# Optimization experiments

Hardware: AMD Instinct MI355X
Metric: run time of the kernel (lower is better)

## Reference

```python
import jax, jax.numpy as jnp
import numpy as np

LAGS = 2
SLOPE = 0.2  # leaky_relu negative slope


def setup_inputs() -> dict:
    key = jax.random.key(0)
    ks = jax.random.split(key, 12)
    B, T, D, E, H = 32, 1002, 16, 32, 64  # batch, lags+length, latent, embed, hidden
    s = 0.1
    return {
        "x": jax.random.normal(ks[0], (B, T, D), jnp.float32),
        "embeddings": jax.random.normal(ks[1], (B, T, E), jnp.float32),
        # per-latent-dim stacked MLP2 params (num_layers=3 hidden + output head)
        "W0": jax.random.normal(ks[2], (D, H, E + 1), jnp.float32) * s,
        "b0": jax.random.normal(ks[3], (D, H), jnp.float32) * s,
        "W1": jax.random.normal(ks[4], (D, H, H), jnp.float32) * s,
        "b1": jax.random.normal(ks[5], (D, H), jnp.float32) * s,
        "W2": jax.random.normal(ks[6], (D, H, H), jnp.float32) * s,
        "b2": jax.random.normal(ks[7], (D, H), jnp.float32) * s,
        "Wo": jax.random.normal(ks[8], (D, 1, H), jnp.float32) * s,
        "bo": jax.random.normal(ks[9], (D, 1), jnp.float32) * s,
    }


def reference(x, embeddings, W0, b0, W1, b1, W2, b2, Wo, bo):
    B, TL, D = x.shape
    length = TL - LAGS
    E = embeddings.shape[-1]
    N = B * length

    # last element of each unfolded window == x[:, LAGS:, :]
    x_t = x[:, LAGS:, :].reshape(N, D)                       # [N, D]
    emb = embeddings[:, -length:, :].reshape(N, E)           # [N, E]
    # per-dim input: concat(embedding, x_t[:, i]) -> [N, D, E+1]
    inp = jnp.concatenate(
        [jnp.broadcast_to(emb[:, None, :], (N, D, E)), x_t[:, :, None]], axis=-1
    )

    # batched tiny MLPs across latent dims; keep leaky-relu gates for analytic Jacobian
    z0 = jnp.einsum('dhe,nde->ndh', W0, inp) + b0            # [N, D, H]
    g0 = jnp.where(z0 >= 0, 1.0, SLOPE)
    a0 = z0 * g0
    z1 = jnp.einsum('dij,ndj->ndi', W1, a0) + b1
    g1 = jnp.where(z1 >= 0, 1.0, SLOPE)
    a1 = z1 * g1
    z2 = jnp.einsum('dij,ndj->ndi', W2, a1) + b2
    g2 = jnp.where(z2 >= 0, 1.0, SLOPE)
    a2 = z2 * g2
    res = jnp.einsum('doh,ndh->ndo', Wo, a2)[..., 0] + bo[:, 0]   # [N, D]

    # d residual_i / d x_t_i : propagate last input column through the chain
    t = g0 * W0[:, :, -1]                                    # [N, D, H]
    t = g1 * jnp.einsum('dij,ndj->ndi', W1, t)
    t = g2 * jnp.einsum('dij,ndj->ndi', W2, t)
    dJ = jnp.einsum('doh,ndh->ndo', Wo, t)[..., 0]           # [N, D]

    logabsdet = jnp.sum(jnp.log(jnp.abs(dJ)), axis=-1)       # [N]

    residuals = res.reshape(B, length, D)
    log_abs_det_jacobian = logabsdet.reshape(B, length)
    return residuals, log_abs_det_jacobian
```

## Files before the change

kernel.cpp:

```cpp
#include <hip/hip_runtime.h>

constexpr int   kT    = 1002;
constexpr int   kD    = 16;
constexpr int   kE    = 32;
constexpr int   kH    = 64;
constexpr int   kLen  = kT - 2;
constexpr int   kN    = 32 * kLen;
constexpr float kSlope = 0.2f;
constexpr int   AS    = 68;
constexpr int   kWsDwPerD = 23552;

typedef __attribute__((ext_vector_type(8))) short bf16x8;
typedef __attribute__((ext_vector_type(4))) float f32x4;
typedef __attribute__((ext_vector_type(2))) __fp16 fp16x2;
typedef __attribute__((ext_vector_type(8))) _Float16 f16x8;

__device__ __forceinline__ unsigned rne2(float x0, float x1, float &h0, float &h1) {
    unsigned u0 = __float_as_uint(x0), u1 = __float_as_uint(x1);
    unsigned r0 = u0 + 0x7FFFu + ((u0 >> 16) & 1u);
    unsigned r1 = u1 + 0x7FFFu + ((u1 >> 16) & 1u);
    h0 = __uint_as_float(r0 & 0xFFFF0000u);
    h1 = __uint_as_float(r1 & 0xFFFF0000u);
    return __builtin_amdgcn_perm(r1, r0, 0x07060302u);
}

__device__ __forceinline__ void split3_2(float x0, float x1,
                                         unsigned &p1, unsigned &p2, unsigned &p3) {
    float h0, h1; p1 = rne2(x0, x1, h0, h1);
    float e0 = x0 - h0, e1 = x1 - h1;
    float m0, m1; p2 = rne2(e0, e1, m0, m1);
    float f0 = e0 - m0, f1 = e1 - m1;
    float t0, t1; p3 = rne2(f0, f1, t0, t1);
}

union FragU { unsigned u[4]; bf16x8 v; };

__device__ __forceinline__ void splitA3(const float4 a0, const float4 a1,
                                        bf16x8 &A1, bf16x8 &A2, bf16x8 &A3) {
    FragU U1, U2, U3;
    split3_2(a0.x, a0.y, U1.u[0], U2.u[0], U3.u[0]);
    split3_2(a0.z, a0.w, U1.u[1], U2.u[1], U3.u[1]);
    split3_2(a1.x, a1.y, U1.u[2], U2.u[2], U3.u[2]);
    split3_2(a1.z, a1.w, U1.u[3], U2.u[3], U3.u[3]);
    A1 = U1.v; A2 = U2.v; A3 = U3.v;
}

__device__ __forceinline__ void split2h(float x0, float x1, unsigned &p1, unsigned &p2) {
    fp16x2 h = __builtin_amdgcn_cvt_pkrtz(x0, x1);
    __builtin_memcpy(&p1, &h, 4);
    fp16x2 l = __builtin_amdgcn_cvt_pkrtz(x0 - (float)h[0], x1 - (float)h[1]);
    __builtin_memcpy(&p2, &l, 4);
}

union FragH { unsigned u[4]; f16x8 v; };

__device__ __forceinline__ void splitA2h(const float4 a0, const float4 a1,
                                         f16x8 &A1, f16x8 &A2) {
    FragH U1, U2;
    split2h(a0.x, a0.y, U1.u[0], U2.u[0]);
    split2h(a0.z, a0.w, U1.u[1], U2.u[1]);
    split2h(a1.x, a1.y, U1.u[2], U2.u[2]);
    split2h(a1.z, a1.w, U1.u[3], U2.u[3]);
    A1 = U1.v; A2 = U2.v;
}

__global__ void prep_weights(const float* __restrict__ W0, const float* __restrict__ W1,
                             const float* __restrict__ W2, unsigned* __restrict__ ws,
                             float* __restrict__ out_ld) {
    int id = blockIdx.x * blockDim.x + threadIdx.x;
    if (id < kN) out_ld[id] = 0.f;
    if (id >= 16 * 9216) return;
    int d = id / 9216, rem = id - d * 9216;
    unsigned* wd = ws + (size_t)d * kWsDwPerD;

    if (rem < 5120) {
        float x0, x1; unsigned o1, o2, o3;
        if (rem < 1024) {
            int idx = rem, j2 = idx & 3, ln = (idx >> 2) & 63, nt = (idx >> 8) & 3;
            int n_ = nt * 16 + (ln & 15), k_ = ((ln >> 4) << 3) + 2 * j2;
            const float* g = W0 + (size_t)d * kH * 33;
            x0 = g[n_ * 33 + k_]; x1 = g[n_ * 33 + k_ + 1];
            o1 = idx; o2 = 1024 + idx; o3 = 2048 + idx;
        } else if (rem < 3072) {
            int idx = rem - 1024, j2 = idx & 3, ln = (idx >> 2) & 63;
            int kt = (idx >> 8) & 1, nt = (idx >> 9) & 3;
            int n_ = nt * 16 + (ln & 15), k_ = kt * 32 + ((ln >> 4) << 3) + 2 * j2;
            const float* g = W1 + (size_t)d * kH * kH;
            x0 = g[n_ * 64 + k_]; x1 = g[n_ * 64 + k_ + 1];
            o1 = 3072 + idx; o2 = 5120 + idx; o3 = 7168 + idx;
        } else {
            int idx = rem - 3072, j2 = idx & 3, ln = (idx >> 2) & 63;
            int kt = (idx >> 8) & 1, nt = (idx >> 9) & 3;
            int n_ = nt * 16 + (ln & 15), k_ = kt * 32 + ((ln >> 4) << 3) + 2 * j2;
            const float* g = W2 + (size_t)d * kH * kH;
            x0 = g[n_ * 64 + k_]; x1 = g[n_ * 64 + k_ + 1];
            o1 = 9216 + idx; o2 = 11264 + idx; o3 = 13312 + idx;
        }
        unsigned p1, p2, p3; split3_2(x0, x1, p1, p2, p3);
        wd[o1] = p1; wd[o2] = p2; wd[o3] = p3;
    } else {
        int idx, base; const float* g;
        if (rem < 7168) { idx = rem - 5120; base = 15360; g = W1 + (size_t)d * kH * kH; }
        else            { idx = rem - 7168; base = 19456; g = W2 + (size_t)d * kH * kH; }
        int j2 = idx & 3, ln = (idx >> 2) & 63;
        int kt = (idx >> 8) & 1, nt = (idx >> 9) & 3;
        int n_ = nt * 16 + (ln & 15), k_ = kt * 32 + ((ln >> 4) << 3) + 2 * j2;
        float x0 = g[n_ * 64 + k_], x1 = g[n_ * 64 + k_ + 1];
        unsigned p1, p2; split2h(x0, x1, p1, p2);
        wd[base + idx] = p1; wd[base + 2048 + idx] = p2;
    }
}

#define MFMA(A, B, C)  __builtin_amdgcn_mfma_f32_16x16x32_bf16((A), (B), (C), 0, 0, 0)
#define MFMAH(A, B, C) __builtin_amdgcn_mfma_f32_16x16x32_f16((A), (B), (C), 0, 0, 0)

__device__ __forceinline__ void layer64_f(f32x4 acc[2][4],
                                          const float* r0, const float* r1,
                                          const unsigned* w1, const unsigned* w2,
                                          const unsigned* w3, int lane, int q) {
    #pragma unroll
    for (int kt = 0; kt < 2; ++kt) {
        bf16x8 A1[2], A2[2], A3[2];
        {
            const float4 a0 = *(const float4*)(r0 + kt * 32 + q * 8);
            const float4 a1 = *(const float4*)(r0 + kt * 32 + q * 8 + 4);
            splitA3(a0, a1, A1[0], A2[0], A3[0]);
            const float4 b0_ = *(const float4*)(r1 + kt * 32 + q * 8);
            const float4 b1_ = *(const float4*)(r1 + kt * 32 + q * 8 + 4);
            splitA3(b0_, b1_, A1[1], A2[1], A3[1]);
        }
        bf16x8 B[4];
        #pragma unroll
        for (int nt = 0; nt < 4; ++nt) B[nt] = *(const bf16x8*)(w1 + (((nt * 2 + kt) * 64 + lane) << 2));
        #pragma unroll
        for (int nt = 0; nt < 4; ++nt)
            #pragma unroll
            for (int mt = 0; mt < 2; ++mt) {
                acc[mt][nt] = MFMA(A3[mt], B[nt], acc[mt][nt]);
                acc[mt][nt] = MFMA(A2[mt], B[nt], acc[mt][nt]);
                acc[mt][nt] = MFMA(A1[mt], B[nt], acc[mt][nt]);
            }
        #pragma unroll
        for (int nt = 0; nt < 4; ++nt) B[nt] = *(const bf16x8*)(w2 + (((nt * 2 + kt) * 64 + lane) << 2));
        #pragma unroll
        for (int nt = 0; nt < 4; ++nt)
            #pragma unroll
            for (int mt = 0; mt < 2; ++mt) {
                acc[mt][nt] = MFMA(A2[mt], B[nt], acc[mt][nt]);
                acc[mt][nt] = MFMA(A1[mt], B[nt], acc[mt][nt]);
            }
        #pragma unroll
        for (int nt = 0; nt < 4; ++nt) B[nt] = *(const bf16x8*)(w3 + (((nt * 2 + kt) * 64 + lane) << 2));
        #pragma unroll
        for (int nt = 0; nt < 4; ++nt)
            #pragma unroll
            for (int mt = 0; mt < 2; ++mt)
                acc[mt][nt] = MFMA(A1[mt], B[nt], acc[mt][nt]);
    }
}

__device__ __forceinline__ void layer64_jh(f32x4 acc[2][4],
                                           const float* r0, const float* r1,
                                           const unsigned* wl1, const unsigned* wl2,
                                           int lane, int q) {
    #pragma unroll
    for (int kt = 0; kt < 2; ++kt) {
        f16x8 A1[2], A2[2];
        {
            const float4 a0 = *(const float4*)(r0 + kt * 32 + q * 8);
            const float4 a1 = *(const float4*)(r0 + kt * 32 + q * 8 + 4);
            splitA2h(a0, a1, A1[0], A2[0]);
            const float4 b0_ = *(const float4*)(r1 + kt * 32 + q * 8);
            const float4 b1_ = *(const float4*)(r1 + kt * 32 + q * 8 + 4);
            splitA2h(b0_, b1_, A1[1], A2[1]);
        }
        f16x8 B[4];
        #pragma unroll
        for (int nt = 0; nt < 4; ++nt) B[nt] = *(const f16x8*)(wl1 + (((nt * 2 + kt) * 64 + lane) << 2));
        #pragma unroll
        for (int nt = 0; nt < 4; ++nt)
            #pragma unroll
            for (int mt = 0; mt < 2; ++mt) {
                acc[mt][nt] = MFMAH(A2[mt], B[nt], acc[mt][nt]);
                acc[mt][nt] = MFMAH(A1[mt], B[nt], acc[mt][nt]);
            }
        #pragma unroll
        for (int nt = 0; nt < 4; ++nt) B[nt] = *(const f16x8*)(wl2 + (((nt * 2 + kt) * 64 + lane) << 2));
        #pragma unroll
        for (int nt = 0; nt < 4; ++nt)
            #pragma unroll
            for (int mt = 0; mt < 2; ++mt)
                acc[mt][nt] = MFMAH(A1[mt], B[nt], acc[mt][nt]);
    }
}

__global__ __launch_bounds__(128, 2) void np_mfma_kernel(
    const float* __restrict__ x, const float* __restrict__ emb,
    const float* __restrict__ W0, const float* __restrict__ b0,
    const float* __restrict__ b1, const float* __restrict__ b2,
    const float* __restrict__ Wo, const float* __restrict__ bo,
    const unsigned* __restrict__ ws,
    float* __restrict__ out_res, float* __restrict__ out_ld)
{
    __shared__ __align__(16) float act[64 * AS];

    const int tid  = threadIdx.x;
    const int lane = tid & 63;
    const int wave = __builtin_amdgcn_readfirstlane(tid >> 6);
    const int c = lane & 15, q = lane >> 4;
    const int tb = wave * 32;
    const int d  = blockIdx.y;
    const int nW = blockIdx.x * 64 + tb;

    const int nX  = nW + ((q >> 1) << 4) + c;
    const int bbX = nX / kLen;
    const float xm = x[((size_t)(bbX * kT + (nX - bbX * kLen) + 2)) * kD + d];
    float xr[2][4];
    #pragma unroll
    for (int mt = 0; mt < 2; ++mt)
        #pragma unroll
        for (int r = 0; r < 4; ++r)
            xr[mt][r] = __shfl(xm, mt * 32 + q * 4 + r, 64);

    const float* W0g = W0 + (size_t)d * kH * 33;
    float b0v[4], wov[4], w0xv[4];
    #pragma unroll
    for (int nt = 0; nt < 4; ++nt) {
        const int u = nt * 16 + c;
        b0v[nt]  = b0[d * kH + u];
        wov[nt]  = Wo[d * kH + u];
        w0xv[nt] = W0g[u * 33 + 32];
    }
    const float bov = bo[d];
    const unsigned* wd = ws + (size_t)d * kWsDwPerD;
    const float* r0 = &act[(tb + c) * AS];
    const float* r1 = &act[(tb + 16 + c) * AS];

    unsigned m0 = 0, m1 = 0, m2 = 0;
    f32x4 acc[2][4];

    {
        bf16x8 A1[2], A2[2], A3[2];
        #pragma unroll
        for (int mt = 0; mt < 2; ++mt) {
            const int nA = nW + mt * 16 + c;
            const int bb = nA / kLen;
            const size_t src = (size_t)(bb * kT + (nA - bb * kLen) + 2);
            const float4* ep = (const float4*)(emb + src * kE + q * 8);
            splitA3(ep[0], ep[1], A1[mt], A2[mt], A3[mt]);
        }
        #pragma unroll
        for (int mt = 0; mt < 2; ++mt)
            #pragma unroll
            for (int nt = 0; nt < 4; ++nt) {
                f32x4 a;
                #pragma unroll
                for (int r = 0; r < 4; ++r) a[r] = fmaf(xr[mt][r], w0xv[nt], b0v[nt]);
                acc[mt][nt] = a;
            }
        bf16x8 B[4];
        #pragma unroll
        for (int nt = 0; nt < 4; ++nt) B[nt] = *(const bf16x8*)(wd + ((nt * 64 + lane) << 2));
        #pragma unroll
        for (int nt = 0; nt < 4; ++nt)
            #pragma unroll
            for (int mt = 0; mt < 2; ++mt) {
                acc[mt][nt] = MFMA(A3[mt], B[nt], acc[mt][nt]);
                acc[mt][nt] = MFMA(A2[mt], B[nt], acc[mt][nt]);
                acc[mt][nt] = MFMA(A1[mt], B[nt], acc[mt][nt]);
            }
        #pragma unroll
        for (int nt = 0; nt < 4; ++nt) B[nt] = *(const bf16x8*)(wd + 1024 + ((nt * 64 + lane) << 2));
        #pragma unroll
        for (int nt = 0; nt < 4; ++nt)
            #pragma unroll
            for (int mt = 0; mt < 2; ++mt) {
                acc[mt][nt] = MFMA(A2[mt], B[nt], acc[mt][nt]);
                acc[mt][nt] = MFMA(A1[mt], B[nt], acc[mt][nt]);
            }
        #pragma unroll
        for (int nt = 0; nt < 4; ++nt) B[nt] = *(const bf16x8*)(wd + 2048 + ((nt * 64 + lane) << 2));
        #pragma unroll
        for (int nt = 0; nt < 4; ++nt)
            #pragma unroll
            for (int mt = 0; mt < 2; ++mt)
                acc[mt][nt] = MFMA(A1[mt], B[nt], acc[mt][nt]);
        #pragma unroll
        for (int mt = 0; mt < 2; ++mt)
            #pragma unroll
            for (int nt = 0; nt < 4; ++nt)
                #pragma unroll
                for (int r = 0; r < 4; ++r) {
                    float z = acc[mt][nt][r];
                    m0 |= (unsigned)(z >= 0.f) << (mt * 16 + nt * 4 + r);
                    act[(tb + mt * 16 + q * 4 + r) * AS + nt * 16 + c] = fmaxf(z, z * kSlope);
                }
    }

    {
        #pragma unroll
        for (int nt = 0; nt < 4; ++nt) {
            const float bv = b1[d * kH + nt * 16 + c];
            #pragma unroll
            for (int mt = 0; mt < 2; ++mt) {
                f32x4 a;
                #pragma unroll
                for (int r = 0; r < 4; ++r) a[r] = bv;
                acc[mt][nt] = a;
            }
        }
        layer64_f(acc, r0, r1, wd + 3072, wd + 5120, wd + 7168, lane, q);
        #pragma unroll
        for (int mt = 0; mt < 2; ++mt)
            #pragma unroll
            for (int nt = 0; nt < 4; ++nt)
                #pragma unroll
                for (int r = 0; r < 4; ++r) {
                    float z = acc[mt][nt][r];
                    m1 |= (unsigned)(z >= 0.f) << (mt * 16 + nt * 4 + r);
                    act[(tb + mt * 16 + q * 4 + r) * AS + nt * 16 + c] = fmaxf(z, z * kSlope);
                }
    }

    {
        #pragma unroll
        for (int nt = 0; nt < 4; ++nt) {
            const float bv = b2[d * kH + nt * 16 + c];
            #pragma unroll
            for (int mt = 0; mt < 2; ++mt) {
                f32x4 a;
                #pragma unroll
                for (int r = 0; r < 4; ++r) a[r] = bv;
                acc[mt][nt] = a;
            }
        }
        layer64_f(acc, r0, r1, wd + 9216, wd + 11264, wd + 13312, lane, q);
        float pr[2][4] = {{0.f,0.f,0.f,0.f},{0.f,0.f,0.f,0.f}};
        #pragma unroll
        for (int mt = 0; mt < 2; ++mt)
            #pragma unroll
            for (int nt = 0; nt < 4; ++nt)
                #pragma unroll
                for (int r = 0; r < 4; ++r) {
                    float z = acc[mt][nt][r];
                    m2 |= (unsigned)(z >= 0.f) << (mt * 16 + nt * 4 + r);
                    pr[mt][r] = fmaf(wov[nt], fmaxf(z, z * kSlope), pr[mt][r]);
                }
        #pragma unroll
        for (int mt = 0; mt < 2; ++mt)
            #pragma unroll
            for (int r = 0; r < 4; ++r) {
                #pragma unroll
                for (int s = 1; s < 16; s <<= 1) pr[mt][r] += __shfl_xor(pr[mt][r], s, 16);
            }
        if (c == 0) {
            #pragma unroll
            for (int mt = 0; mt < 2; ++mt)
                #pragma unroll
                for (int r = 0; r < 4; ++r)
                    out_res[(size_t)(nW + mt * 16 + q * 4 + r) * kD + d] = pr[mt][r] + bov;
        }
    }

    #pragma unroll
    for (int mt = 0; mt < 2; ++mt)
        #pragma unroll
        for (int nt = 0; nt < 4; ++nt)
            #pragma unroll
            for (int r = 0; r < 4; ++r)
                act[(tb + mt * 16 + q * 4 + r) * AS + nt * 16 + c] =
                    (((m0 >> (mt * 16 + nt * 4 + r)) & 1u) ? 1.f : kSlope) * w0xv[nt];

    {
        #pragma unroll
        for (int mt = 0; mt < 2; ++mt)
            #pragma unroll
            for (int nt = 0; nt < 4; ++nt) acc[mt][nt] = (f32x4){0.f, 0.f, 0.f, 0.f};
        layer64_jh(acc, r0, r1, wd + 15360, wd + 17408, lane, q);
        #pragma unroll
        for (int mt = 0; mt < 2; ++mt)
            #pragma unroll
            for (int nt = 0; nt < 4; ++nt)
                #pragma unroll
                for (int r = 0; r < 4; ++r)
                    act[(tb + mt * 16 + q * 4 + r) * AS + nt * 16 + c] =
                        (((m1 >> (mt * 16 + nt * 4 + r)) & 1u) ? 1.f : kSlope) * acc[mt][nt][r];
    }

    {
        #pragma unroll
        for (int mt = 0; mt < 2; ++mt)
            #pragma unroll
            for (int nt = 0; nt < 4; ++nt) acc[mt][nt] = (f32x4){0.f, 0.f, 0.f, 0.f};
        layer64_jh(acc, r0, r1, wd + 19456, wd + 21504, lane, q);
        float pr[2][4] = {{0.f,0.f,0.f,0.f},{0.f,0.f,0.f,0.f}};
        #pragma unroll
        for (int mt = 0; mt < 2; ++mt)
            #pragma unroll
            for (int nt = 0; nt < 4; ++nt)
                #pragma unroll
                for (int r = 0; r < 4; ++r) {
                    float t = (((m2 >> (mt * 16 + nt * 4 + r)) & 1u) ? 1.f : kSlope) * acc[mt][nt][r];
                    pr[mt][r] = fmaf(wov[nt], t, pr[mt][r]);
                }
        #pragma unroll
        for (int mt = 0; mt < 2; ++mt)
            #pragma unroll
            for (int r = 0; r < 4; ++r) {
                #pragma unroll
                for (int s = 1; s < 16; s <<= 1) pr[mt][r] += __shfl_xor(pr[mt][r], s, 16);
            }
        if (c == 0) {
            #pragma unroll
            for (int mt = 0; mt < 2; ++mt)
                #pragma unroll
                for (int r = 0; r < 4; ++r)
                    atomicAdd(&out_ld[nW + mt * 16 + q * 4 + r], __logf(fabsf(pr[mt][r])));
        }
    }
}

extern "C" void kernel_launch(void* const* d_in, const int* in_sizes, int n_in,
                              void* d_out, int out_size, void* d_ws, size_t ws_size,
                              hipStream_t stream) {
    const float* x  = (const float*)d_in[0];
    const float* em = (const float*)d_in[1];
    const float* W0 = (const float*)d_in[2];
    const float* b0 = (const float*)d_in[3];
    const float* W1 = (const float*)d_in[4];
    const float* b1 = (const float*)d_in[5];
    const float* W2 = (const float*)d_in[6];
    const float* b2 = (const float*)d_in[7];
    const float* Wo = (const float*)d_in[8];
    const float* bo = (const float*)d_in[9];

    float* out_res = (float*)d_out;
    float* out_ld  = (float*)d_out + (size_t)kN * kD;
    unsigned* ws   = (unsigned*)d_ws;

    prep_weights<<<dim3(16 * 9216 / 256), dim3(256), 0, stream>>>(W0, W1, W2, ws, out_ld);
    np_mfma_kernel<<<dim3(kN / 64, kD), dim3(128), 0, stream>>>(
        x, em, W0, b0, b1, b2, Wo, bo, ws, out_res, out_ld);
}
```

Measured before the change: 184.8 us.

## Pre-split embeddings into bf16 triples in workspace and truncate activation splits

When the workspace is large enough, the prep kernel now converts each embedding row into three bf16 split components once, instead of having all 16 latent-dim blocks redo the split from fp32. The main kernel then loads those precomputed fragments directly. The in-kernel activation split also switches the first two terms from round-to-nearest to truncation, which saves ALU work while the three-term split keeps overall accuracy. In exchange the prep kernel does more work and there is an extra round trip of about 6 MB through workspace.

```diff
diff --git a/kernel.cpp b/kernel.cpp
--- a/kernel.cpp
+++ b/kernel.cpp
@@ -8,7 +8,12 @@
 constexpr int   kN    = 32 * kLen;
 constexpr float kSlope = 0.2f;
 constexpr int   AS    = 68;
-constexpr int   kWsDwPerD = 23552;
+constexpr int   kWsDwPerD   = 23552;
+constexpr int   kWsEmbBase  = 16 * kWsDwPerD;
+constexpr int   kEmbRowDw   = 48;
+constexpr int   kWsEmbDw    = kN * kEmbRowDw;
+constexpr int   kPrepW      = 16 * 9216;
+constexpr int   kPrepE      = kN * 16;
 
 typedef __attribute__((ext_vector_type(8))) short bf16x8;
 typedef __attribute__((ext_vector_type(4))) float f32x4;
@@ -24,6 +29,13 @@
     return __builtin_amdgcn_perm(r1, r0, 0x07060302u);
 }
 
+__device__ __forceinline__ unsigned trunc2(float x0, float x1, float &h0, float &h1) {
+    unsigned u0 = __float_as_uint(x0), u1 = __float_as_uint(x1);
+    h0 = __uint_as_float(u0 & 0xFFFF0000u);
+    h1 = __uint_as_float(u1 & 0xFFFF0000u);
+    return __builtin_amdgcn_perm(u1, u0, 0x07060302u);
+}
+
 __device__ __forceinline__ void split3_2(float x0, float x1,
                                          unsigned &p1, unsigned &p2, unsigned &p3) {
     float h0, h1; p1 = rne2(x0, x1, h0, h1);
@@ -33,15 +45,24 @@
     float t0, t1; p3 = rne2(f0, f1, t0, t1);
 }
 
+__device__ __forceinline__ void split3t_2(float x0, float x1,
+                                          unsigned &p1, unsigned &p2, unsigned &p3) {
+    float h0, h1; p1 = trunc2(x0, x1, h0, h1);
+    float e0 = x0 - h0, e1 = x1 - h1;
+    float m0, m1; p2 = trunc2(e0, e1, m0, m1);
+    float f0 = e0 - m0, f1 = e1 - m1;
+    float t0, t1; p3 = rne2(f0, f1, t0, t1);
+}
+
 union FragU { unsigned u[4]; bf16x8 v; };
 
-__device__ __forceinline__ void splitA3(const float4 a0, const float4 a1,
-                                        bf16x8 &A1, bf16x8 &A2, bf16x8 &A3) {
+__device__ __forceinline__ void splitA3t(const float4 a0, const float4 a1,
+                                         bf16x8 &A1, bf16x8 &A2, bf16x8 &A3) {
     FragU U1, U2, U3;
-    split3_2(a0.x, a0.y, U1.u[0], U2.u[0], U3.u[0]);
-    split3_2(a0.z, a0.w, U1.u[1], U2.u[1], U3.u[1]);
-    split3_2(a1.x, a1.y, U1.u[2], U2.u[2], U3.u[2]);
-    split3_2(a1.z, a1.w, U1.u[3], U2.u[3], U3.u[3]);
+    split3t_2(a0.x, a0.y, U1.u[0], U2.u[0], U3.u[0]);
+    split3t_2(a0.z, a0.w, U1.u[1], U2.u[1], U3.u[1]);
+    split3t_2(a1.x, a1.y, U1.u[2], U2.u[2], U3.u[2]);
+    split3t_2(a1.z, a1.w, U1.u[3], U2.u[3], U3.u[3]);
     A1 = U1.v; A2 = U2.v; A3 = U3.v;
 }
 
@@ -65,49 +86,59 @@
 }
 
 __global__ void prep_weights(const float* __restrict__ W0, const float* __restrict__ W1,
-                             const float* __restrict__ W2, unsigned* __restrict__ ws,
-                             float* __restrict__ out_ld) {
+                             const float* __restrict__ W2, const float* __restrict__ emb,
+                             unsigned* __restrict__ ws, float* __restrict__ out_ld,
+                             int do_emb) {
     int id = blockIdx.x * blockDim.x + threadIdx.x;
     if (id < kN) out_ld[id] = 0.f;
-    if (id >= 16 * 9216) return;
-    int d = id / 9216, rem = id - d * 9216;
-    unsigned* wd = ws + (size_t)d * kWsDwPerD;
-
-    if (rem < 5120) {
-        float x0, x1; unsigned o1, o2, o3;
-        if (rem < 1024) {
-            int idx = rem, j2 = idx & 3, ln = (idx >> 2) & 63, nt = (idx >> 8) & 3;
-            int n_ = nt * 16 + (ln & 15), k_ = ((ln >> 4) << 3) + 2 * j2;
-            const float* g = W0 + (size_t)d * kH * 33;
-            x0 = g[n_ * 33 + k_]; x1 = g[n_ * 33 + k_ + 1];
-            o1 = idx; o2 = 1024 + idx; o3 = 2048 + idx;
-        } else if (rem < 3072) {
-            int idx = rem - 1024, j2 = idx & 3, ln = (idx >> 2) & 63;
+    if (id < kPrepW) {
+        int d = id / 9216, rem = id - d * 9216;
+        unsigned* wd = ws + (size_t)d * kWsDwPerD;
+        if (rem < 5120) {
+            float x0, x1; unsigned o1, o2, o3;
+            if (rem < 1024) {
+                int idx = rem, j2 = idx & 3, ln = (idx >> 2) & 63, nt = (idx >> 8) & 3;
+                int n_ = nt * 16 + (ln & 15), k_ = ((ln >> 4) << 3) + 2 * j2;
+                const float* g = W0 + (size_t)d * kH * 33;
+                x0 = g[n_ * 33 + k_]; x1 = g[n_ * 33 + k_ + 1];
+                o1 = idx; o2 = 1024 + idx; o3 = 2048 + idx;
+            } else if (rem < 3072) {
+                int idx = rem - 1024, j2 = idx & 3, ln = (idx >> 2) & 63;
+                int kt = (idx >> 8) & 1, nt = (idx >> 9) & 3;
+                int n_ = nt * 16 + (ln & 15), k_ = kt * 32 + ((ln >> 4) << 3) + 2 * j2;
+                const float* g = W1 + (size_t)d * kH * kH;
+                x0 = g[n_ * 64 + k_]; x1 = g[n_ * 64 + k_ + 1];
+                o1 = 3072 + idx; o2 = 5120 + idx; o3 = 7168 + idx;
+            } else {
+                int idx = rem - 3072, j2 = idx & 3, ln = (idx >> 2) & 63;
+                int kt = (idx >> 8) & 1, nt = (idx >> 9) & 3;
+                int n_ = nt * 16 + (ln & 15), k_ = kt * 32 + ((ln >> 4) << 3) + 2 * j2;
+                const float* g = W2 + (size_t)d * kH * kH;
+                x0 = g[n_ * 64 + k_]; x1 = g[n_ * 64 + k_ + 1];
+                o1 = 9216 + idx; o2 = 11264 + idx; o3 = 13312 + idx;
+            }
+            unsigned p1, p2, p3; split3_2(x0, x1, p1, p2, p3);
+            wd[o1] = p1; wd[o2] = p2; wd[o3] = p3;
+        } else {
+            int idx, base; const float* g;
+            if (rem < 7168) { idx = rem - 5120; base = 15360; g = W1 + (size_t)d * kH * kH; }
+            else            { idx = rem - 7168; base = 19456; g = W2 + (size_t)d * kH * kH; }
+            int j2 = idx & 3, ln = (idx >> 2) & 63;
             int kt = (idx >> 8) & 1, nt = (idx >> 9) & 3;
             int n_ = nt * 16 + (ln & 15), k_ = kt * 32 + ((ln >> 4) << 3) + 2 * j2;
-            const float* g = W1 + (size_t)d * kH * kH;
-            x0 = g[n_ * 64 + k_]; x1 = g[n_ * 64 + k_ + 1];
-            o1 = 3072 + idx; o2 = 5120 + idx; o3 = 7168 + idx;
-        } else {
-            int idx = rem - 3072, j2 = idx & 3, ln = (idx >> 2) & 63;
-            int kt = (idx >> 8) & 1, nt = (idx >> 9) & 3;
-            int n_ = nt * 16 + (ln & 15), k_ = kt * 32 + ((ln >> 4) << 3) + 2 * j2;
-            const float* g = W2 + (size_t)d * kH * kH;
-            x0 = g[n_ * 64 + k_]; x1 = g[n_ * 64 + k_ + 1];
-            o1 = 9216 + idx; o2 = 11264 + idx; o3 = 13312 + idx;
-        }
+            float x0 = g[n_ * 64 + k_], x1 = g[n_ * 64 + k_ + 1];
+            unsigned p1, p2; split2h(x0, x1, p1, p2);
+            wd[base + idx] = p1; wd[base + 2048 + idx] = p2;
+        }
+    } else if (do_emb && id < kPrepW + kPrepE) {
+        int eid = id - kPrepW;
+        int n = eid >> 4, p = eid & 15;
+        int bb = n / kLen;
+        size_t src = (size_t)(bb * kT + (n - bb * kLen) + 2);
+        float x0 = emb[src * kE + 2 * p], x1 = emb[src * kE + 2 * p + 1];
         unsigned p1, p2, p3; split3_2(x0, x1, p1, p2, p3);
-        wd[o1] = p1; wd[o2] = p2; wd[o3] = p3;
-    } else {
-        int idx, base; const float* g;
-        if (rem < 7168) { idx = rem - 5120; base = 15360; g = W1 + (size_t)d * kH * kH; }
-        else            { idx = rem - 7168; base = 19456; g = W2 + (size_t)d * kH * kH; }
-        int j2 = idx & 3, ln = (idx >> 2) & 63;
-        int kt = (idx >> 8) & 1, nt = (idx >> 9) & 3;
-        int n_ = nt * 16 + (ln & 15), k_ = kt * 32 + ((ln >> 4) << 3) + 2 * j2;
-        float x0 = g[n_ * 64 + k_], x1 = g[n_ * 64 + k_ + 1];
-        unsigned p1, p2; split2h(x0, x1, p1, p2);
-        wd[base + idx] = p1; wd[base + 2048 + idx] = p2;
+        unsigned* eb = ws + kWsEmbBase + (size_t)n * kEmbRowDw;
+        eb[p] = p1; eb[16 + p] = p2; eb[32 + p] = p3;
     }
 }
 
@@ -124,10 +155,10 @@
         {
             const float4 a0 = *(const float4*)(r0 + kt * 32 + q * 8);
             const float4 a1 = *(const float4*)(r0 + kt * 32 + q * 8 + 4);
-            splitA3(a0, a1, A1[0], A2[0], A3[0]);
+            splitA3t(a0, a1, A1[0], A2[0], A3[0]);
             const float4 b0_ = *(const float4*)(r1 + kt * 32 + q * 8);
             const float4 b1_ = *(const float4*)(r1 + kt * 32 + q * 8 + 4);
-            splitA3(b0_, b1_, A1[1], A2[1], A3[1]);
+            splitA3t(b0_, b1_, A1[1], A2[1], A3[1]);
         }
         bf16x8 B[4];
         #pragma unroll
@@ -199,7 +230,7 @@
     const float* __restrict__ W0, const float* __restrict__ b0,
     const float* __restrict__ b1, const float* __restrict__ b2,
     const float* __restrict__ Wo, const float* __restrict__ bo,
-    const unsigned* __restrict__ ws,
+    const unsigned* __restrict__ ws, const unsigned* __restrict__ embws,
     float* __restrict__ out_res, float* __restrict__ out_ld)
 {
     __shared__ __align__(16) float act[64 * AS];
@@ -241,13 +272,23 @@
 
     {
         bf16x8 A1[2], A2[2], A3[2];
-        #pragma unroll
-        for (int mt = 0; mt < 2; ++mt) {
-            const int nA = nW + mt * 16 + c;
-            const int bb = nA / kLen;
-            const size_t src = (size_t)(bb * kT + (nA - bb * kLen) + 2);
-            const float4* ep = (const float4*)(emb + src * kE + q * 8);
-            splitA3(ep[0], ep[1], A1[mt], A2[mt], A3[mt]);
+        if (embws) {
+            #pragma unroll
+            for (int mt = 0; mt < 2; ++mt) {
+                const unsigned* eb = embws + (size_t)(nW + mt * 16 + c) * kEmbRowDw + q * 4;
+                A1[mt] = *(const bf16x8*)(eb);
+                A2[mt] = *(const bf16x8*)(eb + 16);
+                A3[mt] = *(const bf16x8*)(eb + 32);
+            }
+        } else {
+            #pragma unroll
+            for (int mt = 0; mt < 2; ++mt) {
+                const int nA = nW + mt * 16 + c;
+                const int bb = nA / kLen;
+                const size_t src = (size_t)(bb * kT + (nA - bb * kLen) + 2);
+                const float4* ep = (const float4*)(emb + src * kE + q * 8);
+                splitA3t(ep[0], ep[1], A1[mt], A2[mt], A3[mt]);
+            }
         }
         #pragma unroll
         for (int mt = 0; mt < 2; ++mt)
@@ -438,7 +479,13 @@
     float* out_ld  = (float*)d_out + (size_t)kN * kD;
     unsigned* ws   = (unsigned*)d_ws;
 
-    prep_weights<<<dim3(16 * 9216 / 256), dim3(256), 0, stream>>>(W0, W1, W2, ws, out_ld);
+    const size_t needed = (size_t)(kWsEmbBase + kWsEmbDw) * 4;
+    const bool big = ws_size >= needed;
+    const unsigned* embws = big ? ws + kWsEmbBase : nullptr;
+
+    const int prep_items = big ? (kPrepW + kPrepE) : kPrepW;
+    prep_weights<<<dim3((prep_items + 255) / 256), dim3(256), 0, stream>>>(
+        W0, W1, W2, em, ws, out_ld, big ? 1 : 0);
     np_mfma_kernel<<<dim3(kN / 64, kD), dim3(128), 0, stream>>>(
-        x, em, W0, b0, b1, b2, Wo, bo, ws, out_res, out_ld);
-}
+        x, em, W0, b0, b1, b2, Wo, bo, ws, embws, out_res, out_ld);
+}
```

After: 198.1 us. 1.07x slower.
